# Performance work log

Measured on AMD Instinct MI355X. Metric: run time of the kernel, lower is better.

## Reference

```python
import jax, jax.numpy as jnp
import numpy as np


def setup_inputs() -> dict:
    key = jax.random.key(0)
    k1, k2 = jax.random.split(key)
    B, N, T, D = 16, 2048, 168, 64
    spatial_nodes = jax.random.normal(k1, (B, N, D), dtype=jnp.float32)
    temporal_nodes = jax.random.normal(k2, (B, T, D), dtype=jnp.float32)
    return {"spatial_nodes": spatial_nodes, "temporal_nodes": temporal_nodes}


def reference(spatial_nodes, temporal_nodes):
    # node_embs: [B, N+T, D]
    node_embs = jnp.concatenate([spatial_nodes, temporal_nodes], axis=1)
    # Dense pairwise similarity, then tanh(relu(.)) threshold.
    # batch_adj: [B, N+T, N+T]
    batch_adj = jnp.einsum('bnf,bmf->bnm', node_embs, node_embs)
    batch_adj = jnp.tanh(jax.nn.relu(batch_adj))
    # The torch module additionally extracts per-batch variable-length
    # edge lists (nonzero indices + weights) from batch_adj; those are a
    # pure re-indexing of batch_adj with data-dependent shapes, so the
    # jit-compatible reference returns the dense adjacency, from which
    # edge lists are trivially recoverable (nonzero entries of batch_adj).
    return batch_adj
```

## Files before the change

### kernel.cpp

```cpp
#include <hip/hip_runtime.h>
#include <stdint.h>


constexpr int Bsz = 16;
constexpr int Nsp = 2048;
constexpr int Ttm = 168;
constexpr int D   = 64;
constexpr int M   = Nsp + Ttm;
constexpr int TILE = 128;
constexpr int NT   = (M + TILE - 1) / TILE;
constexpr int NPAIR = NT * (NT + 1) / 2;
constexpr int NG   = NT * 4;
constexpr int GRP_SH   = 4 * 64 * 8;
constexpr int BATCH_SH = NG * GRP_SH;
constexpr int PLANE_SH = Bsz * BATCH_SH;
constexpr size_t WS_NEED = (size_t)2 * PLANE_SH * sizeof(unsigned short);

typedef __attribute__((ext_vector_type(8)))  short bf16x8;
typedef __attribute__((ext_vector_type(16))) float f32x16;

__device__ inline void split8(const float4& a, const float4& b,
                              bf16x8& hi, bf16x8& lo) {
    float x[8] = {a.x, a.y, a.z, a.w, b.x, b.y, b.z, b.w};
    #pragma unroll
    for (int i = 0; i < 8; ++i) {
        union { float f; uint32_t u; } v; v.f = x[i];
        uint32_t hu = (v.u + 0x7FFFu + ((v.u >> 16) & 1u)) >> 16;
        union { uint32_t u; float f; } hf; hf.u = hu << 16;
        union { float f; uint32_t u; } r; r.f = x[i] - hf.f;
        uint32_t lu = (r.u + 0x7FFFu + ((r.u >> 16) & 1u)) >> 16;
        hi[i] = (short)hu;
        lo[i] = (short)lu;
    }
}

__device__ inline float act_tanh_relu(float x) {
    const float xr = fmaxf(x, 0.0f);
    const float e  = __expf(2.0f * xr);
    const float r  = __builtin_amdgcn_rcpf(e + 1.0f);
    return 1.0f - 2.0f * r;
}

__global__ __launch_bounds__(256) void convert_kernel(
    const float* __restrict__ spatial,
    const float* __restrict__ temporal,
    unsigned short* __restrict__ ws)
{
    const int idx = blockIdx.x * 256 + threadIdx.x;
    const int b  = idx / (NG * 4 * 64);
    const int r1 = idx % (NG * 4 * 64);
    const int g  = r1 / (4 * 64);
    const int r2 = r1 % (4 * 64);
    const int ks   = r2 >> 6;
    const int lane = r2 & 63;
    const int row  = 32 * g + (lane & 31);
    const int k0   = ks * 16 + 8 * (lane >> 5);

    float4 v0 = make_float4(0.f, 0.f, 0.f, 0.f), v1 = v0;
    if (row < M) {
        const float* src = (row < Nsp)
            ? spatial  + ((size_t)b * Nsp + row) * D
            : temporal + ((size_t)b * Ttm + (row - Nsp)) * D;
        v0 = *(const float4*)(src + k0);
        v1 = *(const float4*)(src + k0 + 4);
    }
    bf16x8 hi, lo;
    split8(v0, v1, hi, lo);

    const size_t o = (size_t)b * BATCH_SH + (size_t)g * GRP_SH + (ks * 64 + lane) * 8;
    *(bf16x8*)(ws + o)            = hi;
    *(bf16x8*)(ws + PLANE_SH + o) = lo;
}

__global__ __launch_bounds__(256, 4) void stgraph_mfma(
    const unsigned short* __restrict__ ws,
    float* __restrict__ out)
{
    const int tid = threadIdx.x;
    const int b   = blockIdx.y;

    const int p = blockIdx.x;
    int ti = (int)((37.0f - sqrtf(1369.0f - 8.0f * (float)p)) * 0.5f);
    while (ti * (37 - ti) / 2 > p) --ti;
    while ((ti + 1) * (36 - ti) / 2 <= p) ++ti;
    const int tj = ti + (p - ti * (37 - ti) / 2);
    const bool diag = (ti == tj);

    const int lane = tid & 63;
    const int w    = tid >> 6;
    const int l31  = lane & 31;
    const int lhi  = lane >> 5;

    const unsigned short* Hb = ws + (size_t)b * BATCH_SH;
    const unsigned short* Lb = Hb + PLANE_SH;
    const int gA = ti * 4 + w;

    f32x16 acc[4] = {};

    #pragma unroll
    for (int ks = 0; ks < 4; ++ks) {
        const int fo = (ks * 64 + lane) * 8;
        bf16x8 ahi = *(const bf16x8*)(Hb + (size_t)gA * GRP_SH + fo);
        bf16x8 alo = *(const bf16x8*)(Lb + (size_t)gA * GRP_SH + fo);
        #pragma unroll
        for (int t = 0; t < 4; ++t) {
            const int gB = tj * 4 + t;
            bf16x8 bhi = *(const bf16x8*)(Hb + (size_t)gB * GRP_SH + fo);
            bf16x8 blo = *(const bf16x8*)(Lb + (size_t)gB * GRP_SH + fo);
            acc[t] = __builtin_amdgcn_mfma_f32_32x32x16_bf16(ahi, bhi, acc[t], 0, 0, 0);
            acc[t] = __builtin_amdgcn_mfma_f32_32x32x16_bf16(ahi, blo, acc[t], 0, 0, 0);
            acc[t] = __builtin_amdgcn_mfma_f32_32x32x16_bf16(alo, bhi, acc[t], 0, 0, 0);
        }
    }

    float* out_b = out + (size_t)b * M * M;

    #pragma unroll
    for (int t = 0; t < 4; ++t) {
        const int gj = tj * TILE + 32 * t + l31;
        float v[16];
        #pragma unroll
        for (int r = 0; r < 16; ++r) v[r] = act_tanh_relu(acc[t][r]);

        if (gj < M) {
            #pragma unroll
            for (int r = 0; r < 16; ++r) {
                const int gi = ti * TILE + 32 * w + (r & 3) + 8 * (r >> 2) + 4 * lhi;
                if (gi < M) out_b[(size_t)gi * M + gj] = v[r];
            }
            if (!diag) {
                #pragma unroll
                for (int g = 0; g < 4; ++g) {
                    const int gibase = ti * TILE + 32 * w + 8 * g + 4 * lhi;
                    float4 w4 = make_float4(v[4 * g + 0], v[4 * g + 1],
                                            v[4 * g + 2], v[4 * g + 3]);
                    *(float4*)(&out_b[(size_t)gj * M + gibase]) = w4;
                }
            }
        }
    }
}

__global__ __launch_bounds__(256, 3) void stgraph_fallback(
    const float* __restrict__ spatial,
    const float* __restrict__ temporal,
    float* __restrict__ out)
{
    const int tid = threadIdx.x;
    const int b   = blockIdx.y;
    const int p = blockIdx.x;
    int ti = (int)((37.0f - sqrtf(1369.0f - 8.0f * (float)p)) * 0.5f);
    while (ti * (37 - ti) / 2 > p) --ti;
    while ((ti + 1) * (36 - ti) / 2 <= p) ++ti;
    const int tj = ti + (p - ti * (37 - ti) / 2);
    const bool diag = (ti == tj);

    const float* sp_b = spatial  + (size_t)b * Nsp * D;
    const float* tp_b = temporal + (size_t)b * Ttm * D;

    const int lane = tid & 63;
    const int w    = tid >> 6;
    const int l31  = lane & 31;
    const int lhi  = lane >> 5;

    const int giA = ti * TILE + 32 * w + l31;
    const float* rowA = nullptr;
    if (giA < M)
        rowA = (giA < Nsp) ? sp_b + (size_t)giA * D
                           : tp_b + (size_t)(giA - Nsp) * D;
    const float* rowB[4];
    #pragma unroll
    for (int t = 0; t < 4; ++t) {
        const int gj = tj * TILE + 32 * t + l31;
        rowB[t] = nullptr;
        if (gj < M)
            rowB[t] = (gj < Nsp) ? sp_b + (size_t)gj * D
                                 : tp_b + (size_t)(gj - Nsp) * D;
    }

    f32x16 acc[4] = {};
    #pragma unroll
    for (int ks = 0; ks < 4; ++ks) {
        const int ko = ks * 16 + 8 * lhi;
        float4 a0 = make_float4(0.f, 0.f, 0.f, 0.f), a1 = a0;
        if (rowA) { a0 = *(const float4*)(rowA + ko); a1 = *(const float4*)(rowA + ko + 4); }
        bf16x8 ahi, alo;
        split8(a0, a1, ahi, alo);
        #pragma unroll
        for (int t = 0; t < 4; ++t) {
            float4 b0 = make_float4(0.f, 0.f, 0.f, 0.f), b1 = b0;
            if (rowB[t]) { b0 = *(const float4*)(rowB[t] + ko); b1 = *(const float4*)(rowB[t] + ko + 4); }
            bf16x8 bhi, blo;
            split8(b0, b1, bhi, blo);
            acc[t] = __builtin_amdgcn_mfma_f32_32x32x16_bf16(ahi, bhi, acc[t], 0, 0, 0);
            acc[t] = __builtin_amdgcn_mfma_f32_32x32x16_bf16(ahi, blo, acc[t], 0, 0, 0);
            acc[t] = __builtin_amdgcn_mfma_f32_32x32x16_bf16(alo, bhi, acc[t], 0, 0, 0);
        }
    }

    float* out_b = out + (size_t)b * M * M;
    #pragma unroll
    for (int t = 0; t < 4; ++t) {
        const int gj = tj * TILE + 32 * t + l31;
        float v[16];
        #pragma unroll
        for (int r = 0; r < 16; ++r) v[r] = act_tanh_relu(acc[t][r]);
        if (gj < M) {
            #pragma unroll
            for (int r = 0; r < 16; ++r) {
                const int gi = ti * TILE + 32 * w + (r & 3) + 8 * (r >> 2) + 4 * lhi;
                if (gi < M) out_b[(size_t)gi * M + gj] = v[r];
            }
            if (!diag) {
                #pragma unroll
                for (int g = 0; g < 4; ++g) {
                    const int gibase = ti * TILE + 32 * w + 8 * g + 4 * lhi;
                    float4 w4 = make_float4(v[4 * g + 0], v[4 * g + 1],
                                            v[4 * g + 2], v[4 * g + 3]);
                    *(float4*)(&out_b[(size_t)gj * M + gibase]) = w4;
                }
            }
        }
    }
}

extern "C" void kernel_launch(void* const* d_in, const int* in_sizes, int n_in,
                              void* d_out, int out_size, void* d_ws, size_t ws_size,
                              hipStream_t stream) {
    const float* spatial  = (const float*)d_in[0];
    const float* temporal = (const float*)d_in[1];
    float* out = (float*)d_out;

    if (d_ws != nullptr && ws_size >= WS_NEED) {
        unsigned short* ws = (unsigned short*)d_ws;
        {
            dim3 block(256);
            dim3 grid((Bsz * NG * 4 * 64) / 256);
            convert_kernel<<<grid, block, 0, stream>>>(spatial, temporal, ws);
        }
        {
            dim3 block(256);
            dim3 grid(NPAIR, Bsz);
            stgraph_mfma<<<grid, block, 0, stream>>>(ws, out);
        }
    } else {
        dim3 block(256);
        dim3 grid(NPAIR, Bsz);
        stgraph_fallback<<<grid, block, 0, stream>>>(spatial, temporal, out);
    }
}
```

Before: 412.8 us.

## Replace symmetric tile-pair kernel with full row-panel kernel over 32-row groups

Drops the upper-triangular tile-pair scheme, which exploited symmetry by also writing each result transposed. Each block now owns one 32-row panel and its four waves walk all 32-column tiles, computing the full matrix and writing rows contiguously. This removes the strided transposed float4 stores and the triangular index decode. The cost is twice the MFMA work, a smaller grid of NG32 by batch, and a serial loop per wave.

```diff
diff --git a/kernel.cpp b/kernel.cpp
--- a/kernel.cpp
+++ b/kernel.cpp
@@ -7,10 +7,8 @@
 constexpr int Ttm = 168;
 constexpr int D   = 64;
 constexpr int M   = Nsp + Ttm;
-constexpr int TILE = 128;
-constexpr int NT   = (M + TILE - 1) / TILE;
-constexpr int NPAIR = NT * (NT + 1) / 2;
-constexpr int NG   = NT * 4;
+constexpr int NG32 = (M + 31) / 32;
+constexpr int NG   = 72;
 constexpr int GRP_SH   = 4 * 64 * 8;
 constexpr int BATCH_SH = NG * GRP_SH;
 constexpr int PLANE_SH = Bsz * BATCH_SH;
@@ -72,19 +70,13 @@
     *(bf16x8*)(ws + PLANE_SH + o) = lo;
 }
 
-__global__ __launch_bounds__(256, 4) void stgraph_mfma(
+__global__ __launch_bounds__(256, 4) void stgraph_rowpanel(
     const unsigned short* __restrict__ ws,
     float* __restrict__ out)
 {
     const int tid = threadIdx.x;
+    const int g   = blockIdx.x;
     const int b   = blockIdx.y;
-
-    const int p = blockIdx.x;
-    int ti = (int)((37.0f - sqrtf(1369.0f - 8.0f * (float)p)) * 0.5f);
-    while (ti * (37 - ti) / 2 > p) --ti;
-    while ((ti + 1) * (36 - ti) / 2 <= p) ++ti;
-    const int tj = ti + (p - ti * (37 - ti) / 2);
-    const bool diag = (ti == tj);
 
     const int lane = tid & 63;
     const int w    = tid >> 6;
@@ -93,53 +85,44 @@
 
     const unsigned short* Hb = ws + (size_t)b * BATCH_SH;
     const unsigned short* Lb = Hb + PLANE_SH;
-    const int gA = ti * 4 + w;
-
-    f32x16 acc[4] = {};
-
+
+    bf16x8 ahi[4], alo[4];
     #pragma unroll
     for (int ks = 0; ks < 4; ++ks) {
         const int fo = (ks * 64 + lane) * 8;
-        bf16x8 ahi = *(const bf16x8*)(Hb + (size_t)gA * GRP_SH + fo);
-        bf16x8 alo = *(const bf16x8*)(Lb + (size_t)gA * GRP_SH + fo);
+        ahi[ks] = *(const bf16x8*)(Hb + (size_t)g * GRP_SH + fo);
+        alo[ks] = *(const bf16x8*)(Lb + (size_t)g * GRP_SH + fo);
+    }
+
+    float* out_b = out + (size_t)b * M * M;
+
+    for (int ct = w; ct < NG32; ct += 4) {
+        f32x16 acc = {};
         #pragma unroll
-        for (int t = 0; t < 4; ++t) {
-            const int gB = tj * 4 + t;
-            bf16x8 bhi = *(const bf16x8*)(Hb + (size_t)gB * GRP_SH + fo);
-            bf16x8 blo = *(const bf16x8*)(Lb + (size_t)gB * GRP_SH + fo);
-            acc[t] = __builtin_amdgcn_mfma_f32_32x32x16_bf16(ahi, bhi, acc[t], 0, 0, 0);
-            acc[t] = __builtin_amdgcn_mfma_f32_32x32x16_bf16(ahi, blo, acc[t], 0, 0, 0);
-            acc[t] = __builtin_amdgcn_mfma_f32_32x32x16_bf16(alo, bhi, acc[t], 0, 0, 0);
-        }
-    }
-
-    float* out_b = out + (size_t)b * M * M;
-
-    #pragma unroll
-    for (int t = 0; t < 4; ++t) {
-        const int gj = tj * TILE + 32 * t + l31;
-        float v[16];
-        #pragma unroll
-        for (int r = 0; r < 16; ++r) v[r] = act_tanh_relu(acc[t][r]);
-
-        if (gj < M) {
+        for (int ks = 0; ks < 4; ++ks) {
+            const int fo = (ks * 64 + lane) * 8;
+            bf16x8 bhi = *(const bf16x8*)(Hb + (size_t)ct * GRP_SH + fo);
+            bf16x8 blo = *(const bf16x8*)(Lb + (size_t)ct * GRP_SH + fo);
+            acc = __builtin_amdgcn_mfma_f32_32x32x16_bf16(ahi[ks], bhi, acc, 0, 0, 0);
+            acc = __builtin_amdgcn_mfma_f32_32x32x16_bf16(ahi[ks], blo, acc, 0, 0, 0);
+            acc = __builtin_amdgcn_mfma_f32_32x32x16_bf16(alo[ks], bhi, acc, 0, 0, 0);
+        }
+
+        const int col = 32 * ct + l31;
+        if (col < M) {
             #pragma unroll
             for (int r = 0; r < 16; ++r) {
-                const int gi = ti * TILE + 32 * w + (r & 3) + 8 * (r >> 2) + 4 * lhi;
-                if (gi < M) out_b[(size_t)gi * M + gj] = v[r];
+                const int grow = 32 * g + (r & 3) + 8 * (r >> 2) + 4 * lhi;
+                if (grow < M)
+                    out_b[(size_t)grow * M + col] = act_tanh_relu(acc[r]);
             }
-            if (!diag) {
-                #pragma unroll
-                for (int g = 0; g < 4; ++g) {
-                    const int gibase = ti * TILE + 32 * w + 8 * g + 4 * lhi;
-                    float4 w4 = make_float4(v[4 * g + 0], v[4 * g + 1],
-                                            v[4 * g + 2], v[4 * g + 3]);
-                    *(float4*)(&out_b[(size_t)gj * M + gibase]) = w4;
-                }
-            }
-        }
-    }
-}
+        }
+    }
+}
+
+constexpr int TILE = 128;
+constexpr int NT   = (M + TILE - 1) / TILE;
+constexpr int NPAIR = NT * (NT + 1) / 2;
 
 __global__ __launch_bounds__(256, 3) void stgraph_fallback(
     const float* __restrict__ spatial,
@@ -213,10 +196,10 @@
             }
             if (!diag) {
                 #pragma unroll
-                for (int g = 0; g < 4; ++g) {
-                    const int gibase = ti * TILE + 32 * w + 8 * g + 4 * lhi;
-                    float4 w4 = make_float4(v[4 * g + 0], v[4 * g + 1],
-                                            v[4 * g + 2], v[4 * g + 3]);
+                for (int gq = 0; gq < 4; ++gq) {
+                    const int gibase = ti * TILE + 32 * w + 8 * gq + 4 * lhi;
+                    float4 w4 = make_float4(v[4 * gq + 0], v[4 * gq + 1],
+                                            v[4 * gq + 2], v[4 * gq + 3]);
                     *(float4*)(&out_b[(size_t)gj * M + gibase]) = w4;
                 }
             }
@@ -240,8 +223,8 @@
         }
         {
             dim3 block(256);
-            dim3 grid(NPAIR, Bsz);
-            stgraph_mfma<<<grid, block, 0, stream>>>(ws, out);
+            dim3 grid(NG32, Bsz);
+            stgraph_rowpanel<<<grid, block, 0, stream>>>(ws, out);
         }
     } else {
         dim3 block(256);
```

After: 409.7 us. No clear change (-0.8%).
